# Kernel tuning notes

Measured on AMD Instinct MI355X. Metric: run time of the kernel, lower is better.

The kernel has to match this reference:

```python
import jax, jax.numpy as jnp
import numpy as np

WIDTH = 32
DEPTH = 3
B, J, K = 16, 256, 384
C_MODEL, C_OBS, C_META = 1, 1, 6
C_IN = C_MODEL + C_OBS + C_META  # concat channels fed to image_mlp


def _mlp(h, W_stack, b_stack):
    # depth x (Linear -> ReLU) hidden blocks
    for d in range(W_stack.shape[0]):
        h = jax.nn.relu(h @ W_stack[d] + b_stack[d])
    return h


def setup_inputs() -> dict:
    key = jax.random.key(0)
    ks = jax.random.split(key, 14)
    Imodel = jax.random.normal(ks[0], (B, J, K, C_MODEL), jnp.float32)
    Iobs = jax.random.normal(ks[1], (B, J, K, C_OBS), jnp.float32)
    metadata = jax.random.normal(ks[2], (B, J, K, C_META), jnp.float32)
    mask = jax.random.randint(ks[3], (B, J, K, 1), 0, 2) > 0

    def init_w(k, fan_in, fan_out):
        return jax.random.normal(k, (fan_in, fan_out), jnp.float32) / np.sqrt(fan_in)

    params = dict(
        W_img_in=init_w(ks[4], C_IN, WIDTH),
        b_img_in=jnp.zeros((WIDTH,), jnp.float32),
        W_img=jax.random.normal(ks[5], (DEPTH, WIDTH, WIDTH), jnp.float32) / np.sqrt(WIDTH),
        b_img=jnp.zeros((DEPTH, WIDTH), jnp.float32),
        W_lin_in=init_w(ks[6], C_META, WIDTH),
        b_lin_in=jnp.zeros((WIDTH,), jnp.float32),
        W_mlp=jax.random.normal(ks[7], (DEPTH, WIDTH, WIDTH), jnp.float32) / np.sqrt(WIDTH),
        b_mlp=jnp.zeros((DEPTH, WIDTH), jnp.float32),
        W_out=init_w(ks[8], WIDTH, 1),
        b_out=jnp.zeros((1,), jnp.float32),
    )
    return dict(Imodel=Imodel, Iobs=Iobs, metadata=metadata, mask=mask,
                sample_size=32, **params)


def reference(Imodel, Iobs, metadata, mask, sample_size,
              W_img_in, b_img_in, W_img, b_img,
              W_lin_in, b_lin_in, W_mlp, b_mlp, W_out, b_out):
    batch = Iobs.shape[0]
    # p: probability of each image having any observed reflection, normalized
    p = jnp.any(mask, axis=-2)[..., 0].astype(jnp.float32)  # [B, J]
    p = p / jnp.sum(p, axis=-1, keepdims=True)
    # multinomial without replacement via Gumbel top-k (fixed key)
    g = jax.random.gumbel(jax.random.key(42), p.shape, jnp.float32)
    scores = jnp.log(p) + g  # -inf where p == 0, never selected
    _, j = jax.lax.top_k(scores, sample_size)  # [B, S]
    idx = j[:, :, None, None]  # broadcast over K and channel dims

    im = jnp.take_along_axis(Imodel, idx, axis=1)    # [B, S, K, 1]
    io = jnp.take_along_axis(Iobs, idx, axis=1)      # [B, S, K, 1]
    md = jnp.take_along_axis(metadata, idx, axis=1)  # [B, S, K, 6]
    image_data = jnp.concatenate((im, io, md), axis=-1)  # [B, S, K, 8]
    image_mask = jnp.take_along_axis(mask, idx, axis=1).astype(jnp.float32)  # [B, S, K, 1]

    # image_mlp: input linear + depth hidden blocks
    h = image_data @ W_img_in + b_img_in
    h = _mlp(h, W_img, b_img)  # [B, S, K, WIDTH]
    # masked mean over sampled reflections
    image_rep = jnp.sum(image_mask * h, axis=(1, 2), keepdims=True)
    image_rep = image_rep / jnp.sum(image_mask, axis=(1, 2), keepdims=True)  # [B,1,1,WIDTH]

    scale = metadata @ W_lin_in + b_lin_in  # [B, J, K, WIDTH]
    scale = scale + image_rep
    scale = _mlp(scale, W_mlp, b_mlp)
    scale = scale @ W_out + b_out  # [B, J, K, 1]
    return jnp.where(mask, scale, 0.0)
```

## Files before the change

### kernel.cpp

```cpp
#include <hip/hip_runtime.h>
#include <hip/hip_bf16.h>
#include <stdint.h>

#define BB   16
#define JJ   256
#define KK   384
#define NROW (BB * JJ)
#define NPOS ((size_t)BB * JJ * KK)

#define WS_FLAG  0
#define WS_SEL   64
#define WS_VINT  2176
#define WS_VBYTE (WS_VINT + NROW * 4)
#define WS_PART  (WS_VBYTE + NROW * 4)
#define WS_REPB  (WS_PART + 512 * 33 * 4)

typedef float f32x4 __attribute__((ext_vector_type(4)));
typedef short bf16x8 __attribute__((ext_vector_type(8)));

struct FragU { union { bf16x8 v; uint32_t u[4]; }; };

__device__ __forceinline__ uint32_t rotl32(uint32_t x, int r) {
  return (x << r) | (x >> (32 - r));
}

__device__ __forceinline__ void threefry2x32_k42(uint32_t c0, uint32_t c1,
                                                 uint32_t& o0, uint32_t& o1) {
  const uint32_t ks0 = 0u, ks1 = 42u, ks2 = 0x1BD11BDAu ^ 0u ^ 42u;
  uint32_t x0 = c0 + ks0, x1 = c1 + ks1;
#define TFR(r) { x0 += x1; x1 = rotl32(x1, r); x1 ^= x0; }
  TFR(13) TFR(15) TFR(26) TFR(6)   x0 += ks1; x1 += ks2 + 1u;
  TFR(17) TFR(29) TFR(16) TFR(24)  x0 += ks2; x1 += ks0 + 2u;
  TFR(13) TFR(15) TFR(26) TFR(6)   x0 += ks0; x1 += ks1 + 3u;
  TFR(17) TFR(29) TFR(16) TFR(24)  x0 += ks1; x1 += ks2 + 4u;
  TFR(13) TFR(15) TFR(26) TFR(6)   x0 += ks2; x1 += ks0 + 5u;
#undef TFR
  o0 = x0; o1 = x1;
}

__device__ __forceinline__ uint32_t jax_bits(uint32_t t) {
  uint32_t o0, o1;
  threefry2x32_k42(0u, t, o0, o1);
  return o0 ^ o1;
}

__device__ __forceinline__ void split2(float x, short& h, short& l) {
  const unsigned short hu = __builtin_bit_cast(unsigned short, __float2bfloat16(x));
  const float hf = __builtin_bit_cast(float, (uint32_t)hu << 16);
  h = (short)hu;
  l = (short)__builtin_bit_cast(unsigned short, __float2bfloat16(x - hf));
}

__device__ __forceinline__ void split_pk(float x0, float x1,
                                         uint32_t& ph, uint32_t& pl) {
  const uint32_t u0 = __builtin_bit_cast(uint32_t, x0);
  const uint32_t u1 = __builtin_bit_cast(uint32_t, x1);
  ph = __builtin_amdgcn_perm(u1, u0, 0x07060302u);
  const float r0 = x0 - __builtin_bit_cast(float, u0 & 0xFFFF0000u);
  const float r1 = x1 - __builtin_bit_cast(float, u1 & 0xFFFF0000u);
  uint32_t p;
  asm("v_cvt_pk_bf16_f32 %0, %1, %2" : "=v"(p) : "v"(r0), "v"(r1));
  pl = p;
}

__device__ __forceinline__ void refrag_ll(const f32x4 dT0, const f32x4 dT1,
                                          bf16x8& Bh, bf16x8& Bl) {
  FragU H, L;
  split_pk(dT0[0], dT0[1], H.u[0], L.u[0]);
  split_pk(dT0[2], dT0[3], H.u[1], L.u[1]);
  split_pk(dT1[0], dT1[1], H.u[2], L.u[2]);
  split_pk(dT1[2], dT1[3], H.u[3], L.u[3]);
  Bh = H.v; Bl = L.v;
}

__device__ __forceinline__ void refrag_br(f32x4 dT0, f32x4 dT1,
                                          const f32x4 b0, const f32x4 b1,
                                          bf16x8& Bh, bf16x8& Bl) {
#pragma unroll
  for (int r = 0; r < 4; ++r) {
    dT0[r] = fmaxf(dT0[r] + b0[r], 0.f);
    dT1[r] = fmaxf(dT1[r] + b1[r], 0.f);
  }
  refrag_ll(dT0, dT1, Bh, Bl);
}

__global__ __launch_bounds__(256) void k_valid(const void* __restrict__ maskp,
                                               int* __restrict__ valid_int,
                                               int* __restrict__ valid_byte) {
  const int row = blockIdx.x * 4 + (threadIdx.x >> 6);
  const int lane = threadIdx.x & 63;
  const uint32_t* wi = (const uint32_t*)maskp + (size_t)row * 384;
  int v = 0;
#pragma unroll
  for (int i = 0; i < 6; ++i) v |= (wi[lane + i * 64] != 0u);
  const unsigned long long bi = __ballot(v);
  const uint32_t* wb = (const uint32_t*)maskp + (size_t)row * 96;
  int u = 0;
  for (int i = lane; i < 96; i += 64) u |= (wb[i] != 0u);
  const unsigned long long bu = __ballot(u);
  if (lane == 0) {
    valid_int[row] = (bi != 0ull) ? 1 : 0;
    valid_byte[row] = (bu != 0ull) ? 1 : 0;
  }
}

__global__ void k_select(const void* __restrict__ maskp,
                         const int* __restrict__ valid_int,
                         const int* __restrict__ valid_byte,
                         const int* __restrict__ sample_size,
                         int* __restrict__ flag_out, int* __restrict__ sel) {
  const int b = blockIdx.x, lane = threadIdx.x;
  const uint32_t* mw = (const uint32_t*)maskp;
  int big = 0;
#pragma unroll
  for (int i = 0; i < 16; ++i) big |= (mw[lane + i * 64] > 1u);
  const int fl = (__ballot(big) != 0ull) ? 1 : 0;
  if (b == 0 && lane == 0) flag_out[0] = fl;
  const int* valid = fl ? valid_byte : valid_int;

  uint32_t comp[4];
#pragma unroll
  for (int q = 0; q < 4; ++q) {
    const int j = lane * 4 + q;
    const uint32_t ub = jax_bits((uint32_t)(b * 256 + j)) >> 9;
    const uint32_t key = valid[b * 256 + j] ? (ub + 1u) : 0u;
    comp[q] = (key << 8) | (uint32_t)(255 - j);
  }
  int S = sample_size[0];
  if (S > 32) S = 32;
  for (int s = 0; s < S; ++s) {
    uint32_t wm = comp[0];
    wm = comp[1] > wm ? comp[1] : wm;
    wm = comp[2] > wm ? comp[2] : wm;
    wm = comp[3] > wm ? comp[3] : wm;
#pragma unroll
    for (int off = 32; off; off >>= 1) {
      const uint32_t o = __shfl_xor(wm, off);
      wm = o > wm ? o : wm;
    }
    if (wm == 0u) {
      if (lane == 0) sel[b * 32 + s] = 0;
    } else {
#pragma unroll
      for (int q = 0; q < 4; ++q) {
        if (comp[q] == wm) {
          sel[b * 32 + s] = 255 - (int)(comp[q] & 0xFFu);
          comp[q] = 0u;
        }
      }
    }
  }
  for (int s2 = S + lane; s2 < 32; s2 += 64) sel[b * 32 + s2] = 0;
}

__global__ __launch_bounds__(256, 1) void k_image(
    const float* __restrict__ Imodel, const float* __restrict__ Iobs,
    const float* __restrict__ md, const void* __restrict__ maskp,
    const int* __restrict__ flag, const int* __restrict__ sel,
    const int* __restrict__ sample_size,
    const float* __restrict__ W_in, const float* __restrict__ b_in,
    const float* __restrict__ Wd, const float* __restrict__ bd,
    float* __restrict__ partial) {
  __shared__ float red[4 * 33];
  const int tid = threadIdx.x, wid = tid >> 6, lane = tid & 63;
  const int g = lane >> 4, c = lane & 15;
  const int blk = blockIdx.x;
  const int b = blk >> 5, s = blk & 31;
  const bool active = (s < sample_size[0]);
  const int j = sel[b * 32 + s] & 255;
  const size_t pos0 = ((size_t)(b * JJ + j)) * KK + (size_t)wid * 96;
  const int fl = flag[0];

  bf16x8 AWi[2];
#pragma unroll
  for (int ct = 0; ct < 2; ++ct) {
    short bh, bl; split2(b_in[ct * 16 + c], bh, bl);
#pragma unroll
    for (int e = 0; e < 8; ++e) {
      short v;
      if (g <= 1) {
        short hh, ll; split2(W_in[e * 32 + ct * 16 + c], hh, ll);
        v = hh;
      } else if (g == 2) {
        short hh, ll; split2(W_in[e * 32 + ct * 16 + c], hh, ll);
        v = ll;
      } else {
        v = (e == 0) ? bh : ((e == 1) ? bl : (short)0);
      }
      AWi[ct][e] = v;
    }
  }

  bf16x8 AhW[3][2], AlW[3][2];
#pragma unroll
  for (int d = 0; d < 3; ++d)
#pragma unroll
    for (int ct = 0; ct < 2; ++ct)
#pragma unroll
      for (int e = 0; e < 8; ++e) {
        const int f = (e < 4) ? (4 * g + e) : (16 + 4 * g + (e - 4));
        short hh, ll; split2(Wd[d * 1024 + f * 32 + ct * 16 + c], hh, ll);
        AhW[d][ct][e] = hh; AlW[d][ct][e] = ll;
      }
  f32x4 bsA[3], bsB[3];
#pragma unroll
  for (int d = 0; d < 3; ++d)
#pragma unroll
    for (int r = 0; r < 4; ++r) {
      bsA[d][r] = bd[d * 32 + 4 * g + r];
      bsB[d][r] = bd[d * 32 + 16 + 4 * g + r];
    }

  f32x4 acc0 = {0.f, 0.f, 0.f, 0.f}, acc1 = {0.f, 0.f, 0.f, 0.f};
  float cntv = 0.f;
  const f32x4 z = {0.f, 0.f, 0.f, 0.f};

#pragma unroll 2
  for (int t = 0; t < 6; ++t) {
    const size_t tb = pos0 + (size_t)t * 16;
    const size_t p = tb + c;
    const float i0 = Imodel[p];
    const float i1 = Iobs[p];
    const float* mp = md + p * 6;
    const float2 v0 = *(const float2*)(mp);
    const float2 v1 = *(const float2*)(mp + 2);
    const float2 v2 = *(const float2*)(mp + 4);
    float m;
    if (fl) m = (((const uint8_t*)maskp)[p] != 0) ? 1.f : 0.f;
    else    m = (((const int*)maskp)[p] != 0) ? 1.f : 0.f;
    if (!active) m = 0.f;

    uint32_t ph[4], pl[4];
    split_pk(i0, i1, ph[0], pl[0]);
    split_pk(v0.x, v0.y, ph[1], pl[1]);
    split_pk(v1.x, v1.y, ph[2], pl[2]);
    split_pk(v2.x, v2.y, ph[3], pl[3]);
    FragU Bi;
#pragma unroll
    for (int i = 0; i < 4; ++i) {
      const uint32_t t0 = (g == 1) ? pl[i] : ph[i];
      Bi.u[i] = (g == 3) ? ((i == 0) ? 0x3F803F80u : 0u) : t0;
    }

    f32x4 dT0 = __builtin_amdgcn_mfma_f32_16x16x32_bf16(AWi[0], Bi.v, z, 0, 0, 0);
    f32x4 dT1 = __builtin_amdgcn_mfma_f32_16x16x32_bf16(AWi[1], Bi.v, z, 0, 0, 0);
    bf16x8 Bh, Bl;
    refrag_ll(dT0, dT1, Bh, Bl);

#pragma unroll
    for (int d = 0; d < 3; ++d) {
      dT0 = __builtin_amdgcn_mfma_f32_16x16x32_bf16(AhW[d][0], Bh, z, 0, 0, 0);
      dT1 = __builtin_amdgcn_mfma_f32_16x16x32_bf16(AhW[d][1], Bh, z, 0, 0, 0);
      dT0 = __builtin_amdgcn_mfma_f32_16x16x32_bf16(AlW[d][0], Bh, dT0, 0, 0, 0);
      dT1 = __builtin_amdgcn_mfma_f32_16x16x32_bf16(AlW[d][1], Bh, dT1, 0, 0, 0);
      dT0 = __builtin_amdgcn_mfma_f32_16x16x32_bf16(AhW[d][0], Bl, dT0, 0, 0, 0);
      dT1 = __builtin_amdgcn_mfma_f32_16x16x32_bf16(AhW[d][1], Bl, dT1, 0, 0, 0);
      if (d < 2) {
        refrag_br(dT0, dT1, bsA[d], bsB[d], Bh, Bl);
      } else {
#pragma unroll
        for (int r = 0; r < 4; ++r) {
          acc0[r] = fmaf(m, fmaxf(dT0[r] + bsA[2][r], 0.f), acc0[r]);
          acc1[r] = fmaf(m, fmaxf(dT1[r] + bsB[2][r], 0.f), acc1[r]);
        }
        cntv += m;
      }
    }
  }

#pragma unroll
  for (int off = 1; off < 16; off <<= 1) {
#pragma unroll
    for (int r = 0; r < 4; ++r) {
      acc0[r] += __shfl_xor(acc0[r], off);
      acc1[r] += __shfl_xor(acc1[r], off);
    }
    cntv += __shfl_xor(cntv, off);
  }
  if (c == 0) {
#pragma unroll
    for (int r = 0; r < 4; ++r) {
      red[wid * 33 + 4 * g + r] = acc0[r];
      red[wid * 33 + 16 + 4 * g + r] = acc1[r];
    }
    if (g == 0) red[wid * 33 + 32] = cntv;
  }
  __syncthreads();
  if (tid < 33) {
    partial[blk * 33 + tid] =
        red[tid] + red[33 + tid] + red[66 + tid] + red[99 + tid];
  }
}

__global__ void k_rep(const float* __restrict__ partial,
                      const float* __restrict__ b_lin,
                      float* __restrict__ rep_bias) {
  const int b = blockIdx.x, n = threadIdx.x;
  float sum = 0.f, cnt = 0.f;
  for (int s = 0; s < 32; ++s) {
    sum += partial[(b * 32 + s) * 33 + n];
    cnt += partial[(b * 32 + s) * 33 + 32];
  }
  rep_bias[b * 32 + n] = b_lin[n] + sum / cnt;
}

__global__ __launch_bounds__(256, 3) void k_scale(
    const float* __restrict__ md, const void* __restrict__ maskp,
    const int* __restrict__ flag,
    const float* __restrict__ W_lin, const float* __restrict__ rep_bias,
    const float* __restrict__ Wd, const float* __restrict__ bd,
    const float* __restrict__ W_out, const float* __restrict__ b_out,
    float* __restrict__ out) {
  const int tid = threadIdx.x;
  const int wid = tid >> 6, lane = tid & 63;
  const int g = lane >> 4, c = lane & 15;
  const int job = blockIdx.x * 4 + wid;
  const int b = job / 384;
  const size_t pos0 = (size_t)job * 256;
  const int fl = flag[0];
  const bool gLt2 = (g < 2);

  bf16x8 AW[2];
#pragma unroll
  for (int ct = 0; ct < 2; ++ct) {
    const float rb = rep_bias[b * 32 + ct * 16 + c];
    short rbh, rbl; split2(rb, rbh, rbl);
#pragma unroll
    for (int e = 0; e < 8; ++e) {
      short v = 0;
      if (e < 6) {
        short wh, wl; split2(W_lin[e * 32 + ct * 16 + c], wh, wl);
        v = gLt2 ? wh : wl;
      } else if (g == 0) {
        v = (e == 6) ? rbh : rbl;
      }
      AW[ct][e] = v;
    }
  }

  bf16x8 AhW[3][2], AlW[3][2];
#pragma unroll
  for (int d = 0; d < 3; ++d)
#pragma unroll
    for (int ct = 0; ct < 2; ++ct)
#pragma unroll
      for (int e = 0; e < 8; ++e) {
        const int f = (e < 4) ? (4 * g + e) : (16 + 4 * g + (e - 4));
        short hh, ll; split2(Wd[d * 1024 + f * 32 + ct * 16 + c], hh, ll);
        AhW[d][ct][e] = hh; AlW[d][ct][e] = ll;
      }
  f32x4 bsA[3], bsB[3];
#pragma unroll
  for (int d = 0; d < 3; ++d)
#pragma unroll
    for (int r = 0; r < 4; ++r) {
      bsA[d][r] = bd[d * 32 + 4 * g + r];
      bsB[d][r] = bd[d * 32 + 16 + 4 * g + r];
    }
  f32x4 woA, woB;
#pragma unroll
  for (int r = 0; r < 4; ++r) {
    woA[r] = W_out[4 * g + r];
    woB[r] = W_out[16 + 4 * g + r];
  }
  const float bo = b_out[0];
  const uint32_t bias_word = (g == 0) ? 0x00003F80u : 0u;
  const f32x4 z = {0.f, 0.f, 0.f, 0.f};

  const float* mdp = md + (pos0 + c) * 6;
  const uint8_t* mb8 = (const uint8_t*)maskp + pos0 + c;
  const uint32_t* mb32 = (const uint32_t*)maskp + pos0 + c;

#pragma unroll 4
  for (int t = 0; t < 16; ++t) {
    const size_t tb = pos0 + (size_t)t * 16;

    const float* mrow = mdp + t * 96;
    const float2 a01 = *(const float2*)(mrow);
    const float2 a23 = *(const float2*)(mrow + 2);
    const float2 a45 = *(const float2*)(mrow + 4);
    uint32_t mk;
    if (fl) mk = (uint32_t)mb8[t * 16];
    else    mk = mb32[t * 16];

    FragU Bin;
    {
      uint32_t ph0, pl0, ph1, pl1, ph2, pl2;
      split_pk(a01.x, a01.y, ph0, pl0);
      split_pk(a23.x, a23.y, ph1, pl1);
      split_pk(a45.x, a45.y, ph2, pl2);
      Bin.u[0] = (g & 1) ? pl0 : ph0;
      Bin.u[1] = (g & 1) ? pl1 : ph1;
      Bin.u[2] = (g & 1) ? pl2 : ph2;
      Bin.u[3] = bias_word;
    }

    f32x4 dT0 = __builtin_amdgcn_mfma_f32_16x16x32_bf16(AW[0], Bin.v, z, 0, 0, 0);
    f32x4 dT1 = __builtin_amdgcn_mfma_f32_16x16x32_bf16(AW[1], Bin.v, z, 0, 0, 0);

    bf16x8 Bh, Bl;
    refrag_ll(dT0, dT1, Bh, Bl);

#pragma unroll
    for (int d = 0; d < 3; ++d) {
      dT0 = __builtin_amdgcn_mfma_f32_16x16x32_bf16(AhW[d][0], Bh, z, 0, 0, 0);
      dT1 = __builtin_amdgcn_mfma_f32_16x16x32_bf16(AhW[d][1], Bh, z, 0, 0, 0);
      dT0 = __builtin_amdgcn_mfma_f32_16x16x32_bf16(AlW[d][0], Bh, dT0, 0, 0, 0);
      dT1 = __builtin_amdgcn_mfma_f32_16x16x32_bf16(AlW[d][1], Bh, dT1, 0, 0, 0);
      dT0 = __builtin_amdgcn_mfma_f32_16x16x32_bf16(AhW[d][0], Bl, dT0, 0, 0, 0);
      dT1 = __builtin_amdgcn_mfma_f32_16x16x32_bf16(AhW[d][1], Bl, dT1, 0, 0, 0);
      if (d < 2) {
        refrag_br(dT0, dT1, bsA[d], bsB[d], Bh, Bl);
      } else {
        float sum = 0.f;
#pragma unroll
        for (int r = 0; r < 4; ++r) {
          sum = fmaf(fmaxf(dT0[r] + bsA[2][r], 0.f), woA[r], sum);
          sum = fmaf(fmaxf(dT1[r] + bsB[2][r], 0.f), woB[r], sum);
        }
        sum += __shfl_xor(sum, 16);
        sum += __shfl_xor(sum, 32);
        if (g == 0) out[tb + c] = mk ? (sum + bo) : 0.0f;
      }
    }
  }
}

extern "C" void kernel_launch(void* const* d_in, const int* in_sizes, int n_in,
                              void* d_out, int out_size, void* d_ws, size_t ws_size,
                              hipStream_t stream) {
  const float* Imodel   = (const float*)d_in[0];
  const float* Iobs     = (const float*)d_in[1];
  const float* metadata = (const float*)d_in[2];
  const void*  mask     = d_in[3];
  const int*   sample_size = (const int*)d_in[4];
  const float* W_img_in = (const float*)d_in[5];
  const float* b_img_in = (const float*)d_in[6];
  const float* W_img    = (const float*)d_in[7];
  const float* b_img    = (const float*)d_in[8];
  const float* W_lin_in = (const float*)d_in[9];
  const float* b_lin_in = (const float*)d_in[10];
  const float* W_mlp    = (const float*)d_in[11];
  const float* b_mlp    = (const float*)d_in[12];
  const float* W_out    = (const float*)d_in[13];
  const float* b_out    = (const float*)d_in[14];
  float* out = (float*)d_out;

  char* ws = (char*)d_ws;
  int*   flag     = (int*)(ws + WS_FLAG);
  int*   sel      = (int*)(ws + WS_SEL);
  int*   vint     = (int*)(ws + WS_VINT);
  int*   vbyte    = (int*)(ws + WS_VBYTE);
  float* partial  = (float*)(ws + WS_PART);
  float* rep_bias = (float*)(ws + WS_REPB);

  k_valid<<<NROW / 4, 256, 0, stream>>>(mask, vint, vbyte);
  k_select<<<BB, 64, 0, stream>>>(mask, vint, vbyte, sample_size, flag, sel);
  k_image<<<512, 256, 0, stream>>>(Imodel, Iobs, metadata, mask, flag, sel,
                                   sample_size, W_img_in, b_img_in, W_img,
                                   b_img, partial);
  k_rep<<<BB, 32, 0, stream>>>(partial, b_lin_in, rep_bias);
  k_scale<<<1536, 256, 0, stream>>>(metadata, mask, flag, W_lin_in, rep_bias,
                                    W_mlp, b_mlp, W_out, b_out, out);
}
```

Measured before the change: 82.99 us.

## Switch scale MLP to 32x32x16 MFMA with register-resident refragmentation and prefetch

Rewrites the per-position scale MLP in k_scale to use 32x32x16 bf16 MFMAs, so each wave handles 32 positions per iteration instead of 16. The operand layout is chosen so the accumulator output can be split into hi/lo bf16 B-fragments directly in registers, which removes the cross-lane refrag shuffles and one xor-shuffle in the final reduction. It also software-prefetches the next tile's metadata and mask values and lowers launch_bounds occupancy from 3 to 2 to make room for the larger accumulators. The risks are higher register pressure and lower occupancy, which reduce latency hiding.

```diff
diff --git a/kernel.cpp b/kernel.cpp
--- a/kernel.cpp
+++ b/kernel.cpp
@@ -16,6 +16,7 @@
 #define WS_REPB  (WS_PART + 512 * 33 * 4)
 
 typedef float f32x4 __attribute__((ext_vector_type(4)));
+typedef float f32x16 __attribute__((ext_vector_type(16)));
 typedef short bf16x8 __attribute__((ext_vector_type(8)));
 
 struct FragU { union { bf16x8 v; uint32_t u[4]; }; };
@@ -304,7 +305,7 @@
   rep_bias[b * 32 + n] = b_lin[n] + sum / cnt;
 }
 
-__global__ __launch_bounds__(256, 3) void k_scale(
+__global__ __launch_bounds__(256, 2) void k_scale(
     const float* __restrict__ md, const void* __restrict__ maskp,
     const int* __restrict__ flag,
     const float* __restrict__ W_lin, const float* __restrict__ rep_bias,
@@ -313,116 +314,136 @@
     float* __restrict__ out) {
   const int tid = threadIdx.x;
   const int wid = tid >> 6, lane = tid & 63;
-  const int g = lane >> 4, c = lane & 15;
+  const int p = lane & 31, h = lane >> 5;
   const int job = blockIdx.x * 4 + wid;
   const int b = job / 384;
   const size_t pos0 = (size_t)job * 256;
   const int fl = flag[0];
-  const bool gLt2 = (g < 2);
-
-  bf16x8 AW[2];
-#pragma unroll
-  for (int ct = 0; ct < 2; ++ct) {
-    const float rb = rep_bias[b * 32 + ct * 16 + c];
-    short rbh, rbl; split2(rb, rbh, rbl);
+
+  bf16x8 AW;
+  {
+    short rbh, rbl; split2(rep_bias[b * 32 + p], rbh, rbl);
 #pragma unroll
     for (int e = 0; e < 8; ++e) {
       short v = 0;
       if (e < 6) {
-        short wh, wl; split2(W_lin[e * 32 + ct * 16 + c], wh, wl);
-        v = gLt2 ? wh : wl;
-      } else if (g == 0) {
+        short wh, wl; split2(W_lin[e * 32 + p], wh, wl);
+        v = h ? wl : wh;
+      } else if (h == 0) {
         v = (e == 6) ? rbh : rbl;
       }
-      AW[ct][e] = v;
-    }
-  }
-
-  bf16x8 AhW[3][2], AlW[3][2];
+      AW[e] = v;
+    }
+  }
+
+  bf16x8 Ah[3][2], Al[3][2];
 #pragma unroll
   for (int d = 0; d < 3; ++d)
 #pragma unroll
-    for (int ct = 0; ct < 2; ++ct)
+    for (int m = 0; m < 2; ++m)
 #pragma unroll
       for (int e = 0; e < 8; ++e) {
-        const int f = (e < 4) ? (4 * g + e) : (16 + 4 * g + (e - 4));
-        short hh, ll; split2(Wd[d * 1024 + f * 32 + ct * 16 + c], hh, ll);
-        AhW[d][ct][e] = hh; AlW[d][ct][e] = ll;
-      }
-  f32x4 bsA[3], bsB[3];
-#pragma unroll
-  for (int d = 0; d < 3; ++d)
+        const int f = ((e < 4) ? e : (e + 4)) + 4 * h + 16 * m;
+        short hh, ll; split2(Wd[d * 1024 + f * 32 + p], hh, ll);
+        Ah[d][m][e] = hh; Al[d][m][e] = ll;
+      }
+  f32x4 bs[3][4], wo[4];
+#pragma unroll
+  for (int q4 = 0; q4 < 4; ++q4)
 #pragma unroll
     for (int r = 0; r < 4; ++r) {
-      bsA[d][r] = bd[d * 32 + 4 * g + r];
-      bsB[d][r] = bd[d * 32 + 16 + 4 * g + r];
-    }
-  f32x4 woA, woB;
-#pragma unroll
-  for (int r = 0; r < 4; ++r) {
-    woA[r] = W_out[4 * g + r];
-    woB[r] = W_out[16 + 4 * g + r];
-  }
+      const int f = r + 8 * q4 + 4 * h;
+#pragma unroll
+      for (int d = 0; d < 3; ++d) bs[d][q4][r] = bd[d * 32 + f];
+      wo[q4][r] = W_out[f];
+    }
   const float bo = b_out[0];
-  const uint32_t bias_word = (g == 0) ? 0x00003F80u : 0u;
-  const f32x4 z = {0.f, 0.f, 0.f, 0.f};
-
-  const float* mdp = md + (pos0 + c) * 6;
-  const uint8_t* mb8 = (const uint8_t*)maskp + pos0 + c;
-  const uint32_t* mb32 = (const uint32_t*)maskp + pos0 + c;
-
-#pragma unroll 4
-  for (int t = 0; t < 16; ++t) {
-    const size_t tb = pos0 + (size_t)t * 16;
-
-    const float* mrow = mdp + t * 96;
-    const float2 a01 = *(const float2*)(mrow);
-    const float2 a23 = *(const float2*)(mrow + 2);
-    const float2 a45 = *(const float2*)(mrow + 4);
-    uint32_t mk;
-    if (fl) mk = (uint32_t)mb8[t * 16];
-    else    mk = mb32[t * 16];
-
-    FragU Bin;
+  const uint32_t ones_word = (h == 0) ? 0x3F803F80u : 0u;
+
+  const float* mdp = md + (pos0 + p) * 6;
+  const uint8_t* mb8 = (const uint8_t*)maskp + pos0 + p;
+  const uint32_t* mb32 = (const uint32_t*)maskp + pos0 + p;
+  const f32x16 z16 = {0.f,0.f,0.f,0.f,0.f,0.f,0.f,0.f,
+                      0.f,0.f,0.f,0.f,0.f,0.f,0.f,0.f};
+
+  float2 a01 = *(const float2*)(mdp);
+  float2 a23 = *(const float2*)(mdp + 2);
+  float2 a45 = *(const float2*)(mdp + 4);
+  uint32_t mk = fl ? (uint32_t)mb8[0] : mb32[0];
+
+  for (int t = 0; t < 8; ++t) {
+    const size_t tb = pos0 + (size_t)t * 32;
+
+    float2 n01 = {0.f, 0.f}, n23 = {0.f, 0.f}, n45 = {0.f, 0.f};
+    uint32_t nk = 0;
+    if (t < 7) {
+      const float* nr = mdp + (t + 1) * 192;
+      n01 = *(const float2*)(nr);
+      n23 = *(const float2*)(nr + 2);
+      n45 = *(const float2*)(nr + 4);
+      nk = fl ? (uint32_t)mb8[(t + 1) * 32] : mb32[(t + 1) * 32];
+    }
+
+    FragU B1, B2;
     {
       uint32_t ph0, pl0, ph1, pl1, ph2, pl2;
       split_pk(a01.x, a01.y, ph0, pl0);
       split_pk(a23.x, a23.y, ph1, pl1);
       split_pk(a45.x, a45.y, ph2, pl2);
-      Bin.u[0] = (g & 1) ? pl0 : ph0;
-      Bin.u[1] = (g & 1) ? pl1 : ph1;
-      Bin.u[2] = (g & 1) ? pl2 : ph2;
-      Bin.u[3] = bias_word;
-    }
-
-    f32x4 dT0 = __builtin_amdgcn_mfma_f32_16x16x32_bf16(AW[0], Bin.v, z, 0, 0, 0);
-    f32x4 dT1 = __builtin_amdgcn_mfma_f32_16x16x32_bf16(AW[1], Bin.v, z, 0, 0, 0);
-
-    bf16x8 Bh, Bl;
-    refrag_ll(dT0, dT1, Bh, Bl);
+      B1.u[0] = ph0; B1.u[1] = ph1; B1.u[2] = ph2; B1.u[3] = ones_word;
+      B2.u[0] = pl0; B2.u[1] = pl1; B2.u[2] = pl2; B2.u[3] = 0u;
+    }
+
+    f32x16 dT = __builtin_amdgcn_mfma_f32_32x32x16_bf16(AW, B1.v, z16, 0, 0, 0);
+    dT = __builtin_amdgcn_mfma_f32_32x32x16_bf16(AW, B2.v, dT, 0, 0, 0);
+
+    FragU HA, LA, HB, LB;
+    split_pk(dT[0], dT[1], HA.u[0], LA.u[0]);
+    split_pk(dT[2], dT[3], HA.u[1], LA.u[1]);
+    split_pk(dT[4], dT[5], HA.u[2], LA.u[2]);
+    split_pk(dT[6], dT[7], HA.u[3], LA.u[3]);
+    split_pk(dT[8], dT[9], HB.u[0], LB.u[0]);
+    split_pk(dT[10], dT[11], HB.u[1], LB.u[1]);
+    split_pk(dT[12], dT[13], HB.u[2], LB.u[2]);
+    split_pk(dT[14], dT[15], HB.u[3], LB.u[3]);
 
 #pragma unroll
     for (int d = 0; d < 3; ++d) {
-      dT0 = __builtin_amdgcn_mfma_f32_16x16x32_bf16(AhW[d][0], Bh, z, 0, 0, 0);
-      dT1 = __builtin_amdgcn_mfma_f32_16x16x32_bf16(AhW[d][1], Bh, z, 0, 0, 0);
-      dT0 = __builtin_amdgcn_mfma_f32_16x16x32_bf16(AlW[d][0], Bh, dT0, 0, 0, 0);
-      dT1 = __builtin_amdgcn_mfma_f32_16x16x32_bf16(AlW[d][1], Bh, dT1, 0, 0, 0);
-      dT0 = __builtin_amdgcn_mfma_f32_16x16x32_bf16(AhW[d][0], Bl, dT0, 0, 0, 0);
-      dT1 = __builtin_amdgcn_mfma_f32_16x16x32_bf16(AhW[d][1], Bl, dT1, 0, 0, 0);
+      f32x16 nT = __builtin_amdgcn_mfma_f32_32x32x16_bf16(Ah[d][0], HA.v, z16, 0, 0, 0);
+      nT = __builtin_amdgcn_mfma_f32_32x32x16_bf16(Ah[d][1], HB.v, nT, 0, 0, 0);
+      nT = __builtin_amdgcn_mfma_f32_32x32x16_bf16(Al[d][0], HA.v, nT, 0, 0, 0);
+      nT = __builtin_amdgcn_mfma_f32_32x32x16_bf16(Al[d][1], HB.v, nT, 0, 0, 0);
+      nT = __builtin_amdgcn_mfma_f32_32x32x16_bf16(Ah[d][0], LA.v, nT, 0, 0, 0);
+      nT = __builtin_amdgcn_mfma_f32_32x32x16_bf16(Ah[d][1], LB.v, nT, 0, 0, 0);
       if (d < 2) {
-        refrag_br(dT0, dT1, bsA[d], bsB[d], Bh, Bl);
+        float x[16];
+#pragma unroll
+        for (int q4 = 0; q4 < 4; ++q4)
+#pragma unroll
+          for (int r = 0; r < 4; ++r)
+            x[q4 * 4 + r] = fmaxf(nT[q4 * 4 + r] + bs[d][q4][r], 0.f);
+        split_pk(x[0], x[1], HA.u[0], LA.u[0]);
+        split_pk(x[2], x[3], HA.u[1], LA.u[1]);
+        split_pk(x[4], x[5], HA.u[2], LA.u[2]);
+        split_pk(x[6], x[7], HA.u[3], LA.u[3]);
+        split_pk(x[8], x[9], HB.u[0], LB.u[0]);
+        split_pk(x[10], x[11], HB.u[1], LB.u[1]);
+        split_pk(x[12], x[13], HB.u[2], LB.u[2]);
+        split_pk(x[14], x[15], HB.u[3], LB.u[3]);
       } else {
         float sum = 0.f;
 #pragma unroll
-        for (int r = 0; r < 4; ++r) {
-          sum = fmaf(fmaxf(dT0[r] + bsA[2][r], 0.f), woA[r], sum);
-          sum = fmaf(fmaxf(dT1[r] + bsB[2][r], 0.f), woB[r], sum);
-        }
-        sum += __shfl_xor(sum, 16);
+        for (int q4 = 0; q4 < 4; ++q4)
+#pragma unroll
+          for (int r = 0; r < 4; ++r)
+            sum = fmaf(fmaxf(nT[q4 * 4 + r] + bs[2][q4][r], 0.f),
+                       wo[q4][r], sum);
         sum += __shfl_xor(sum, 32);
-        if (g == 0) out[tb + c] = mk ? (sum + bo) : 0.0f;
-      }
-    }
+        if (h == 0) out[tb + p] = mk ? (sum + bo) : 0.0f;
+      }
+    }
+
+    a01 = n01; a23 = n23; a45 = n45; mk = nk;
   }
 }
 
```

After: 80.66 us. 2.8% less time.
